# Kernel optimization log

Measured on AMD Instinct MI355X. Metric: run time of the kernel, lower is better.

Reference implementation:

```python
import jax, jax.numpy as jnp
import numpy as np

DIM = 768
HEADS = 12
HEAD_DIM = DIM // HEADS
SCALE = HEAD_DIM ** -0.5


def setup_inputs() -> dict:
    key = jax.random.key(0)
    ks = jax.random.split(key, 6)
    B, N, C = 2, 2048, DIM
    x = jax.random.normal(ks[0], (B, N, C), dtype=jnp.float32)
    s = C ** -0.5
    Wq = jax.random.normal(ks[1], (C, C), dtype=jnp.float32) * s
    Wk = jax.random.normal(ks[2], (C, C), dtype=jnp.float32) * s
    Wv = jax.random.normal(ks[3], (C, C), dtype=jnp.float32) * s
    Wp = jax.random.normal(ks[4], (C, C), dtype=jnp.float32) * s
    bp = jax.random.normal(ks[5], (C,), dtype=jnp.float32) * 0.01
    return {"x": x, "Wq": Wq, "Wk": Wk, "Wv": Wv, "Wp": Wp, "bp": bp}


def reference(x, Wq, Wk, Wv, Wp, bp):
    B, N, C = x.shape
    h, d = HEADS, HEAD_DIM
    # projections (no bias), split heads: (B, h, N, d)
    Q = (x @ Wq.T).reshape(B, N, h, d).transpose(0, 2, 1, 3)
    K = (x @ Wk.T).reshape(B, N, h, d).transpose(0, 2, 1, 3)
    V = (x @ Wv.T).reshape(B, N, h, d).transpose(0, 2, 1, 3)
    # averaged key: (B, h, 1, d) -> scores (B, h, N)
    K_avg = K.mean(axis=2)  # (B, h, d)
    z = jnp.einsum('bhnd,bhd->bhn', Q, K_avg) * SCALE
    attn = jax.nn.softmax(z, axis=-1)  # (B, h, N)
    # circulant gather: roll[b,h,i,j] = attn[b,h,(j-i)%N] / N
    idx = (jnp.arange(N)[None, :] - jnp.arange(N)[:, None]) % N  # (N, N)
    roll = attn[:, :, idx] / N  # (B, h, N, N)
    out = jnp.einsum('bhij,bhjd->bhid', roll, V)  # (B, h, N, d)
    out = out.transpose(0, 2, 1, 3).reshape(B, N, C)
    return out @ Wp.T + bp
```

## Files before the change

### kernel.cpp

```cpp
#include <hip/hip_runtime.h>


typedef __bf16 bf16x8 __attribute__((ext_vector_type(8)));
typedef float  f32x4  __attribute__((ext_vector_type(4)));

#define AS_GLOBAL(p) ((const __attribute__((address_space(1))) unsigned int*)(p))
#define AS_LDS(p)    ((__attribute__((address_space(3))) unsigned int*)(p))

__device__ __forceinline__ void async16(const void* g, void* l) {
    __builtin_amdgcn_global_load_lds(AS_GLOBAL(g), AS_LDS(l), 16, 0, 0);
}

struct bf4 { __bf16 a, b, c, d; };

template <int BM, int BN, int MODE>
__device__ void gemm_phase(char* smem, const __bf16* __restrict__ A,
                           const __bf16* __restrict__ Bt, void* __restrict__ Cout,
                           const float* __restrict__ bias,
                           int K, int ldA, int ldBt, int ldC, int mBase, int nBase)
{
    constexpr int BK = 64;
    constexpr int STRIDE = (BM + BN) * BK * 2;
    constexpr int WM = BM / 2, WN = BN / 2;
    constexpr int MI = WM / 16, NI = WN / 16;
    const int tid = threadIdx.x;
    const int lane = tid & 63, wid = tid >> 6;
    const int lane15 = lane & 15, quad = lane >> 4;
    const int wm = (wid & 1) * WM, wn = (wid >> 1) * WN;

    auto stage = [&](int kb, int buf) {
        __bf16* As = (__bf16*)(smem + buf * STRIDE);
        __bf16* Bs = As + BM * BK;
#pragma unroll
        for (int c0 = 0; c0 < BM * 8; c0 += 256) {
            int c = c0 + tid, row = c >> 3, slot = c & 7;
            int k8 = slot ^ (row & 7);
            async16(A + (size_t)(mBase + row) * ldA + kb + k8 * 8, As + c * 8);
        }
#pragma unroll
        for (int c0 = 0; c0 < BN * 8; c0 += 256) {
            int c = c0 + tid, row = c >> 3, slot = c & 7;
            int k8 = slot ^ (row & 7);
            async16(Bt + (size_t)(nBase + row) * ldBt + kb + k8 * 8, Bs + c * 8);
        }
    };

    f32x4 acc[MI][NI] = {};
    const int nk = K >> 6;

    stage(0, 0);
    for (int ki = 0; ki < nk; ++ki) {
        __syncthreads();
        if (ki + 1 < nk) stage((ki + 1) << 6, (ki + 1) & 1);

        __bf16* As = (__bf16*)(smem + (ki & 1) * STRIDE);
        __bf16* Bs = As + BM * BK;
#pragma unroll
        for (int ks = 0; ks < 2; ++ks) {
            bf16x8 af[MI], bv[NI];
#pragma unroll
            for (int mi = 0; mi < MI; ++mi) {
                int row = wm + mi * 16 + lane15;
                af[mi] = *(const bf16x8*)&As[row * 64 + ((ks * 4 + quad) ^ (row & 7)) * 8];
            }
#pragma unroll
            for (int ni = 0; ni < NI; ++ni) {
                int row = wn + ni * 16 + lane15;
                bv[ni] = *(const bf16x8*)&Bs[row * 64 + ((ks * 4 + quad) ^ (row & 7)) * 8];
            }
#pragma unroll
            for (int mi = 0; mi < MI; ++mi)
#pragma unroll
                for (int ni = 0; ni < NI; ++ni)
                    acc[mi][ni] = __builtin_amdgcn_mfma_f32_16x16x32_bf16(
                        af[mi], bv[ni], acc[mi][ni], 0, 0, 0);
        }
    }

#pragma unroll
    for (int mi = 0; mi < MI; ++mi)
#pragma unroll
        for (int ni = 0; ni < NI; ++ni)
#pragma unroll
            for (int r = 0; r < 4; ++r) {
                int row = mBase + wm + mi * 16 + quad * 4 + r;
                int col = nBase + wn + ni * 16 + lane15;
                float v = acc[mi][ni][r];
                if (MODE == 0) {
                    ((__bf16*)Cout)[(size_t)row * ldC + col] = (__bf16)v;
                } else {
                    ((float*)Cout)[(size_t)row * ldC + col] = v + bias[col];
                }
            }
}

__global__ __launch_bounds__(256)
void k_prep(const float* __restrict__ x, const float* __restrict__ Wv,
            const float* __restrict__ Wp,
            __bf16* __restrict__ xb, __bf16* __restrict__ Wvb,
            __bf16* __restrict__ Wpb, float* __restrict__ x_part)
{
    const int bid = blockIdx.x, tid = threadIdx.x;

    const float4* xs = (const float4*)x + (size_t)bid * 1536;
    bf4* xd = (bf4*)xb + (size_t)bid * 1536;
#pragma unroll
    for (int r = 0; r < 6; ++r) {
        int j = tid + r * 256;
        float4 v = xs[j];
        xd[j] = bf4{(__bf16)v.x, (__bf16)v.y, (__bf16)v.z, (__bf16)v.w};
    }
    const float4* wv4 = (const float4*)Wv;  bf4* wvb4 = (bf4*)Wvb;
    const float4* wp4 = (const float4*)Wp;  bf4* wpb4 = (bf4*)Wpb;
    for (int t = tid; t < 288; t += 256) {
        int g = bid * 288 + t;
        float4 v = wv4[g];
        wvb4[g] = bf4{(__bf16)v.x, (__bf16)v.y, (__bf16)v.z, (__bf16)v.w};
        float4 w2 = wp4[g];
        wpb4[g] = bf4{(__bf16)w2.x, (__bf16)w2.y, (__bf16)w2.z, (__bf16)w2.w};
    }

    if (bid < 64) {
        const float* base = x + (size_t)bid * 64 * 768;
        float s0 = 0.f, s1 = 0.f, s2 = 0.f;
        for (int r = 0; r < 64; ++r) {
            const float* row = base + r * 768;
            s0 += row[tid];
            s1 += row[tid + 256];
            s2 += row[tid + 512];
        }
        x_part[bid * 768 + tid]       = s0;
        x_part[bid * 768 + tid + 256] = s1;
        x_part[bid * 768 + tid + 512] = s2;
    }
}

__global__ __launch_bounds__(256, 2)
void k_mid(const __bf16* __restrict__ xb, const __bf16* __restrict__ Wvb,
           const float* __restrict__ x_part, const float* __restrict__ Wk,
           const float* __restrict__ Wq,
           __bf16* __restrict__ VT, float* __restrict__ z_t)
{
    __shared__ __attribute__((aligned(16))) char smem[65536];
    const int bid = blockIdx.x;
    if (bid < 192) {
        gemm_phase<128, 128, 0>(smem, Wvb, xb, VT, nullptr, 768, 768, 768, 4096,
                                (bid / 32) * 128, (bid % 32) * 128);
        return;
    }
    const int tid = threadIdx.x;
    const int lane = tid & 63, wid = tid >> 6;
    const int idx = bid - 192;
    const int bh = idx >> 2, q = idx & 3;
    const int b = bh / 12, h = bh % 12;
    float* xa  = (float*)smem;
    float* uld = xa + 768;
    float* ka  = uld + 768;

    for (int c = tid; c < 768; c += 256) {
        float s = 0.f;
#pragma unroll
        for (int g = 0; g < 32; ++g) s += x_part[(b * 32 + g) * 768 + c];
        xa[c] = s;
    }
    __syncthreads();
    for (int round = 0; round < 16; ++round) {
        int o = round * 4 + wid;
        const float* wk = Wk + (size_t)(h * 64 + o) * 768;
        float s = 0.f;
#pragma unroll
        for (int c0 = 0; c0 < 768; c0 += 64) s += xa[c0 + lane] * wk[c0 + lane];
#pragma unroll
        for (int off = 32; off; off >>= 1) s += __shfl_down(s, off);
        if (lane == 0) ka[o] = s * (0.125f / 2048.f);
    }
    __syncthreads();
    for (int c = tid; c < 768; c += 256) {
        float s = 0.f;
#pragma unroll 16
        for (int d = 0; d < 64; ++d)
            s += ka[d] * Wq[(size_t)(h * 64 + d) * 768 + c];
        uld[c] = s;
    }
    __syncthreads();
    const int t0 = q * 512 + tid, t1 = t0 + 256;
    const bf16x8* r0 = (const bf16x8*)(xb + (size_t)(b * 2048 + t0) * 768);
    const bf16x8* r1 = (const bf16x8*)(xb + (size_t)(b * 2048 + t1) * 768);
    const float4* u4 = (const float4*)uld;
    float s0 = 0.f, s1 = 0.f;
#pragma unroll 8
    for (int j = 0; j < 96; ++j) {
        bf16x8 v0 = r0[j], v1 = r1[j];
        float4 ua = u4[j * 2], ub = u4[j * 2 + 1];
        s0 += (float)v0[0] * ua.x + (float)v0[1] * ua.y + (float)v0[2] * ua.z
            + (float)v0[3] * ua.w + (float)v0[4] * ub.x + (float)v0[5] * ub.y
            + (float)v0[6] * ub.z + (float)v0[7] * ub.w;
        s1 += (float)v1[0] * ua.x + (float)v1[1] * ua.y + (float)v1[2] * ua.z
            + (float)v1[3] * ua.w + (float)v1[4] * ub.x + (float)v1[5] * ub.y
            + (float)v1[6] * ub.z + (float)v1[7] * ub.w;
    }
    z_t[(size_t)bh * 2048 + t0] = s0;
    z_t[(size_t)bh * 2048 + t1] = s1;
}

__global__ __launch_bounds__(256, 2)
void k_conv(const float* __restrict__ z_t, const __bf16* __restrict__ VT,
            __bf16* __restrict__ outp)
{
    __shared__ __attribute__((aligned(16))) char smem[69760];
    __bf16 (*rep)[2056] = (__bf16(*)[2056])smem;
    float* red = (float*)(smem + 32896);
    __bf16* attn_s = (__bf16*)(smem + 65664);

    const int bid = blockIdx.x, tid = threadIdx.x;
    const int lane = tid & 63, wid = tid >> 6;
    const int lane15 = lane & 15, quad = lane >> 4;
    const int bh = bid >> 4, b = bh / 12, h = bh % 12;
    const int m0 = (bid & 15) * 128 + (wid & 1) * 64;
    const int wn = (wid >> 1) * 32;

    {
        const float* z = z_t + (size_t)bh * 2048;
        float v[8];
        float m = -1e30f;
#pragma unroll
        for (int j = 0; j < 8; ++j) { v[j] = z[tid + j * 256]; m = fmaxf(m, v[j]); }
#pragma unroll
        for (int off = 32; off; off >>= 1) m = fmaxf(m, __shfl_xor(m, off));
        if (lane == 0) red[wid] = m;
        __syncthreads();
        m = fmaxf(fmaxf(red[0], red[1]), fmaxf(red[2], red[3]));
        __syncthreads();
        float s = 0.f;
#pragma unroll
        for (int j = 0; j < 8; ++j) { v[j] = __expf(v[j] - m); s += v[j]; }
#pragma unroll
        for (int off = 32; off; off >>= 1) s += __shfl_xor(s, off);
        if (lane == 0) red[wid] = s;
        __syncthreads();
        s = red[0] + red[1] + red[2] + red[3];
        float inv = 1.f / (s * 2048.f);
#pragma unroll
        for (int j = 0; j < 8; ++j)
            attn_s[tid + j * 256] = (__bf16)(v[j] * inv);
    }
    __syncthreads();
    for (int idx = tid; idx < 8 * 2048; idx += 256) {
        int a = idx >> 11, u = idx & 2047;
        rep[a][u] = attn_s[(u + a) & 2047];
    }

    const __bf16* vsrc = VT + (size_t)h * 64 * 4096 + b * 2048;

    auto stage = [&](int kb, int buf) {
        __bf16* vt = (__bf16*)(smem + 32896 + buf * 16384);
#pragma unroll
        for (int c0 = 0; c0 < 1024; c0 += 256) {
            int c = c0 + tid, dd = c >> 4, slot = c & 15;
            int k8 = slot ^ (dd & 15);
            async16(vsrc + (size_t)dd * 4096 + kb * 128 + k8 * 8, vt + c * 8);
        }
    };

    f32x4 acc[4][2] = {};
    stage(0, 0);
    for (int kb = 0; kb < 16; ++kb) {
        __syncthreads();
        if (kb + 1 < 16) stage(kb + 1, (kb + 1) & 1);
        __bf16* vt = (__bf16*)(smem + 32896 + (kb & 1) * 16384);

#pragma unroll
        for (int ks = 0; ks < 4; ++ks) {
            int kloc = ks * 32 + quad * 8;
            int kglob = kb * 128 + kloc;
            bf16x8 af[4], bv[2];
#pragma unroll
            for (int mi = 0; mi < 4; ++mi) {
                int m = m0 + mi * 16 + lane15;
                int p = (kglob - m) & 2047;
                int al = p & 7;
                af[mi] = *(const bf16x8*)&rep[al][p - al];
            }
#pragma unroll
            for (int ni = 0; ni < 2; ++ni) {
                int dd = wn + ni * 16 + lane15;
                int slot = (ks * 4 + quad) ^ (dd & 15);
                bv[ni] = *(const bf16x8*)&vt[dd * 128 + slot * 8];
            }
#pragma unroll
            for (int mi = 0; mi < 4; ++mi)
#pragma unroll
                for (int ni = 0; ni < 2; ++ni)
                    acc[mi][ni] = __builtin_amdgcn_mfma_f32_16x16x32_bf16(
                        af[mi], bv[ni], acc[mi][ni], 0, 0, 0);
        }
    }

#pragma unroll
    for (int mi = 0; mi < 4; ++mi)
#pragma unroll
        for (int ni = 0; ni < 2; ++ni)
#pragma unroll
            for (int r = 0; r < 4; ++r) {
                int i = m0 + mi * 16 + quad * 4 + r;
                int dd = wn + ni * 16 + lane15;
                outp[(size_t)(b * 2048 + i) * 768 + h * 64 + dd] =
                    (__bf16)acc[mi][ni][r];
            }
}

__global__ __launch_bounds__(256, 2)
void k_out(const __bf16* __restrict__ out_pre, const __bf16* __restrict__ Wpb,
           const float* __restrict__ bp, float* __restrict__ out)
{
    __shared__ __attribute__((aligned(16))) char smem[65536];
    const int bid = blockIdx.x;
    gemm_phase<128, 128, 1>(smem, out_pre, Wpb, out, bp, 768, 768, 768, 768,
                            (bid / 6) * 128, (bid % 6) * 128);
}

extern "C" void kernel_launch(void* const* d_in, const int* in_sizes, int n_in,
                              void* d_out, int out_size, void* d_ws, size_t ws_size,
                              hipStream_t stream)
{
    (void)in_sizes; (void)n_in; (void)out_size; (void)ws_size;
    const float* x  = (const float*)d_in[0];
    const float* Wq = (const float*)d_in[1];
    const float* Wk = (const float*)d_in[2];
    const float* Wv = (const float*)d_in[3];
    const float* Wp = (const float*)d_in[4];
    const float* bp = (const float*)d_in[5];

    char* w = (char*)d_ws;
    auto alloc = [&](size_t bytes) {
        char* p = w; w += (bytes + 255) & ~(size_t)255; return p;
    };
    float*  x_part  = (float*) alloc((size_t)64 * 768 * 4);
    __bf16* xb      = (__bf16*)alloc((size_t)4096 * 768 * 2);
    __bf16* Wvb     = (__bf16*)alloc((size_t)768 * 768 * 2);
    __bf16* Wpb     = (__bf16*)alloc((size_t)768 * 768 * 2);
    float*  z_t     = (float*) alloc((size_t)24 * 2048 * 4);
    __bf16* VT      = (__bf16*)alloc((size_t)768 * 4096 * 2);
    __bf16* out_pre = (__bf16*)alloc((size_t)4096 * 768 * 2);

    k_prep<<<512, 256, 0, stream>>>(x, Wv, Wp, xb, Wvb, Wpb, x_part);
    k_mid <<<288, 256, 0, stream>>>(xb, Wvb, x_part, Wk, Wq, VT, z_t);
    k_conv<<<384, 256, 0, stream>>>(z_t, VT, out_pre);
    k_out <<<192, 256, 0, stream>>>(out_pre, Wpb, bp, (float*)d_out);
}
```

Measured before the change: 157.6 us.

## Triple-buffer GEMM and conv tile loads with explicit vmcnt waits and raw barriers

Replaces the double-buffered async global-to-LDS pipeline in the projection GEMMs and the circulant conv kernel with a three-buffer ring. Each iteration waits on vmcnt for only the oldest stage and issues a raw s_barrier, keeping two loads in flight instead of one. The conv kernel's V tile is halved to 64 k per stage, so three buffers fit in a smaller LDS footprint, and the LDS regions are rearranged to match. The GEMM kernels grow to 96KB of LDS, which may reduce occupancy. The raw barrier and hand-counted vmcnt values also depend on the exact number of outstanding loads per stage.

```diff
diff --git a/kernel.cpp b/kernel.cpp
--- a/kernel.cpp
+++ b/kernel.cpp
@@ -11,25 +11,26 @@
     __builtin_amdgcn_global_load_lds(AS_GLOBAL(g), AS_LDS(l), 16, 0, 0);
 }
 
+#define WAITVM(N) asm volatile("s_waitcnt vmcnt(" #N ")" ::: "memory")
+#define RAW_BARRIER() asm volatile("s_barrier" ::: "memory")
+
 struct bf4 { __bf16 a, b, c, d; };
 
-template <int BM, int BN, int MODE>
+template <int MODE>
 __device__ void gemm_phase(char* smem, const __bf16* __restrict__ A,
                            const __bf16* __restrict__ Bt, void* __restrict__ Cout,
                            const float* __restrict__ bias,
                            int K, int ldA, int ldBt, int ldC, int mBase, int nBase)
 {
-    constexpr int BK = 64;
-    constexpr int STRIDE = (BM + BN) * BK * 2;
-    constexpr int WM = BM / 2, WN = BN / 2;
-    constexpr int MI = WM / 16, NI = WN / 16;
+    constexpr int BM = 128, BN = 128, BK = 64;
+    constexpr int BUF = (BM + BN) * BK * 2;
     const int tid = threadIdx.x;
     const int lane = tid & 63, wid = tid >> 6;
     const int lane15 = lane & 15, quad = lane >> 4;
-    const int wm = (wid & 1) * WM, wn = (wid >> 1) * WN;
-
-    auto stage = [&](int kb, int buf) {
-        __bf16* As = (__bf16*)(smem + buf * STRIDE);
+    const int wm = (wid & 1) * 64, wn = (wid >> 1) * 64;
+
+    auto stage = [&](int kb, char* buf) {
+        __bf16* As = (__bf16*)buf;
         __bf16* Bs = As + BM * BK;
 #pragma unroll
         for (int c0 = 0; c0 < BM * 8; c0 += 256) {
@@ -45,42 +46,48 @@
         }
     };
 
-    f32x4 acc[MI][NI] = {};
+    f32x4 acc[4][4] = {};
     const int nk = K >> 6;
-
-    stage(0, 0);
+    char* p0 = smem;
+    char* p1 = smem + BUF;
+    char* p2 = smem + 2 * BUF;
+
+    stage(0, p0);
+    stage(64, p1);
     for (int ki = 0; ki < nk; ++ki) {
-        __syncthreads();
-        if (ki + 1 < nk) stage((ki + 1) << 6, (ki + 1) & 1);
-
-        __bf16* As = (__bf16*)(smem + (ki & 1) * STRIDE);
+        if (ki + 1 < nk) { WAITVM(8); } else { WAITVM(0); }
+        RAW_BARRIER();
+        if (ki + 2 < nk) stage((ki + 2) << 6, p2);
+
+        __bf16* As = (__bf16*)p0;
         __bf16* Bs = As + BM * BK;
 #pragma unroll
         for (int ks = 0; ks < 2; ++ks) {
-            bf16x8 af[MI], bv[NI];
-#pragma unroll
-            for (int mi = 0; mi < MI; ++mi) {
+            bf16x8 af[4], bv[4];
+#pragma unroll
+            for (int mi = 0; mi < 4; ++mi) {
                 int row = wm + mi * 16 + lane15;
                 af[mi] = *(const bf16x8*)&As[row * 64 + ((ks * 4 + quad) ^ (row & 7)) * 8];
             }
 #pragma unroll
-            for (int ni = 0; ni < NI; ++ni) {
+            for (int ni = 0; ni < 4; ++ni) {
                 int row = wn + ni * 16 + lane15;
                 bv[ni] = *(const bf16x8*)&Bs[row * 64 + ((ks * 4 + quad) ^ (row & 7)) * 8];
             }
 #pragma unroll
-            for (int mi = 0; mi < MI; ++mi)
-#pragma unroll
-                for (int ni = 0; ni < NI; ++ni)
+            for (int mi = 0; mi < 4; ++mi)
+#pragma unroll
+                for (int ni = 0; ni < 4; ++ni)
                     acc[mi][ni] = __builtin_amdgcn_mfma_f32_16x16x32_bf16(
                         af[mi], bv[ni], acc[mi][ni], 0, 0, 0);
         }
-    }
-
-#pragma unroll
-    for (int mi = 0; mi < MI; ++mi)
-#pragma unroll
-        for (int ni = 0; ni < NI; ++ni)
+        char* t = p0; p0 = p1; p1 = p2; p2 = t;
+    }
+
+#pragma unroll
+    for (int mi = 0; mi < 4; ++mi)
+#pragma unroll
+        for (int ni = 0; ni < 4; ++ni)
 #pragma unroll
             for (int r = 0; r < 4; ++r) {
                 int row = mBase + wm + mi * 16 + quad * 4 + r;
@@ -141,11 +148,11 @@
            const float* __restrict__ Wq,
            __bf16* __restrict__ VT, float* __restrict__ z_t)
 {
-    __shared__ __attribute__((aligned(16))) char smem[65536];
+    __shared__ __attribute__((aligned(16))) char smem[98304];
     const int bid = blockIdx.x;
     if (bid < 192) {
-        gemm_phase<128, 128, 0>(smem, Wvb, xb, VT, nullptr, 768, 768, 768, 4096,
-                                (bid / 32) * 128, (bid % 32) * 128);
+        gemm_phase<0>(smem, Wvb, xb, VT, nullptr, 768, 768, 768, 4096,
+                      (bid / 32) * 128, (bid % 32) * 128);
         return;
     }
     const int tid = threadIdx.x;
@@ -207,10 +214,10 @@
 void k_conv(const float* __restrict__ z_t, const __bf16* __restrict__ VT,
             __bf16* __restrict__ outp)
 {
-    __shared__ __attribute__((aligned(16))) char smem[69760];
+    __shared__ __attribute__((aligned(16))) char smem[61568];
     __bf16 (*rep)[2056] = (__bf16(*)[2056])smem;
-    float* red = (float*)(smem + 32896);
-    __bf16* attn_s = (__bf16*)(smem + 65664);
+    __bf16* attn_s = (__bf16*)(smem + 32896);
+    float* red = (float*)(smem + 36992);
 
     const int bid = blockIdx.x, tid = threadIdx.x;
     const int lane = tid & 63, wid = tid >> 6;
@@ -249,30 +256,36 @@
         int a = idx >> 11, u = idx & 2047;
         rep[a][u] = attn_s[(u + a) & 2047];
     }
+    __syncthreads();
 
     const __bf16* vsrc = VT + (size_t)h * 64 * 4096 + b * 2048;
 
-    auto stage = [&](int kb, int buf) {
-        __bf16* vt = (__bf16*)(smem + 32896 + buf * 16384);
-#pragma unroll
-        for (int c0 = 0; c0 < 1024; c0 += 256) {
-            int c = c0 + tid, dd = c >> 4, slot = c & 15;
-            int k8 = slot ^ (dd & 15);
-            async16(vsrc + (size_t)dd * 4096 + kb * 128 + k8 * 8, vt + c * 8);
+    auto stage = [&](int kb, char* buf) {
+        __bf16* vt = (__bf16*)buf;
+#pragma unroll
+        for (int c0 = 0; c0 < 512; c0 += 256) {
+            int c = c0 + tid, dd = c >> 3, slot = c & 7;
+            int k8 = slot ^ (dd & 7);
+            async16(vsrc + (size_t)dd * 4096 + kb * 64 + k8 * 8, vt + c * 8);
         }
     };
 
     f32x4 acc[4][2] = {};
-    stage(0, 0);
-    for (int kb = 0; kb < 16; ++kb) {
-        __syncthreads();
-        if (kb + 1 < 16) stage(kb + 1, (kb + 1) & 1);
-        __bf16* vt = (__bf16*)(smem + 32896 + (kb & 1) * 16384);
-
-#pragma unroll
-        for (int ks = 0; ks < 4; ++ks) {
+    char* p0 = smem + 36992;
+    char* p1 = p0 + 8192;
+    char* p2 = p1 + 8192;
+    stage(0, p0);
+    stage(1, p1);
+    for (int kb = 0; kb < 32; ++kb) {
+        if (kb + 1 < 32) { WAITVM(2); } else { WAITVM(0); }
+        RAW_BARRIER();
+        if (kb + 2 < 32) stage(kb + 2, p2);
+        __bf16* vt = (__bf16*)p0;
+
+#pragma unroll
+        for (int ks = 0; ks < 2; ++ks) {
             int kloc = ks * 32 + quad * 8;
-            int kglob = kb * 128 + kloc;
+            int kglob = kb * 64 + kloc;
             bf16x8 af[4], bv[2];
 #pragma unroll
             for (int mi = 0; mi < 4; ++mi) {
@@ -284,8 +297,8 @@
 #pragma unroll
             for (int ni = 0; ni < 2; ++ni) {
                 int dd = wn + ni * 16 + lane15;
-                int slot = (ks * 4 + quad) ^ (dd & 15);
-                bv[ni] = *(const bf16x8*)&vt[dd * 128 + slot * 8];
+                int slot = (ks * 4 + quad) ^ (dd & 7);
+                bv[ni] = *(const bf16x8*)&vt[dd * 64 + slot * 8];
             }
 #pragma unroll
             for (int mi = 0; mi < 4; ++mi)
@@ -294,6 +307,7 @@
                     acc[mi][ni] = __builtin_amdgcn_mfma_f32_16x16x32_bf16(
                         af[mi], bv[ni], acc[mi][ni], 0, 0, 0);
         }
+        char* t = p0; p0 = p1; p1 = p2; p2 = t;
     }
 
 #pragma unroll
@@ -313,10 +327,10 @@
 void k_out(const __bf16* __restrict__ out_pre, const __bf16* __restrict__ Wpb,
            const float* __restrict__ bp, float* __restrict__ out)
 {
-    __shared__ __attribute__((aligned(16))) char smem[65536];
+    __shared__ __attribute__((aligned(16))) char smem[98304];
     const int bid = blockIdx.x;
-    gemm_phase<128, 128, 1>(smem, out_pre, Wpb, out, bp, 768, 768, 768, 768,
-                            (bid / 6) * 128, (bid % 6) * 128);
+    gemm_phase<1>(smem, out_pre, Wpb, out, bp, 768, 768, 768, 768,
+                  (bid / 6) * 128, (bid % 6) * 128);
 }
 
 extern "C" void kernel_launch(void* const* d_in, const int* in_sizes, int n_in,
```

Result: no change. 159.6 us (+1.3%).
